# Kernel optimization log

Hardware: AMD Instinct MI355X
Metric: run time of the kernel (lower is better)

Reference implementation:

```python
import jax, jax.numpy as jnp
import numpy as np

COLOR_SIZE = 8
FILTERS = 128
L = 256 * 256 * 3  # flattened sequence length
EPS = 1e-12  # tf.math.l2_normalize epsilon


def setup_inputs() -> dict:
    key = jax.random.key(0)
    k1, k2, k3, k4, k5, k6 = jax.random.split(key, 6)
    example = jax.random.randint(k1, (4, 256, 256, 3), 0, COLOR_SIZE, dtype=jnp.int32)
    W_in = jax.random.normal(k2, (1, FILTERS), dtype=jnp.float32) * 0.05
    b_in = jnp.zeros((FILTERS,), dtype=jnp.float32)
    pos = jax.random.normal(k3, (L, FILTERS), dtype=jnp.float32) * 0.05
    W_final = jax.random.normal(k4, (FILTERS, COLOR_SIZE), dtype=jnp.float32) * 0.05
    b_final = jnp.zeros((COLOR_SIZE,), dtype=jnp.float32)
    return {"example": example, "W_in": W_in, "b_in": b_in, "pos": pos,
            "W_final": W_final, "b_final": b_final}


def reference(example, W_in, b_in, pos, W_final, b_final):
    B = example.shape[0]
    # cast + rescale to [-1, 1) (applied twice in the original code)
    x = example.astype(jnp.float32) / COLOR_SIZE * 2.0 - 1.0
    x = x.reshape(B, L, 1)
    x = x * 2.0 - 1.0
    # layer 0: Dense(1->F) + positional encoding + relu
    x = x * W_in[0] + b_in + pos  # [B, L, F]
    x = jax.nn.relu(x)
    # causal cumsum over sequence, then l2-normalize feature dim
    s = jnp.cumsum(x, axis=-2)  # [B, L, F]
    x = s * jax.lax.rsqrt(jnp.maximum(jnp.sum(s * s, axis=-1, keepdims=True), EPS))
    # final Dense(F->color_size)
    x = jnp.einsum('blf,fc->blc', x, W_final) + b_final
    return x.reshape(B, 256, 256, 3, COLOR_SIZE)
```

## Files before the change

### kernel.cpp

```cpp
#include <hip/hip_runtime.h>
#include <hip/hip_fp16.h>

#define BB   4
#define FF   128
#define CC   8
#define LSEQ 196608
#define NCH  2048
#define CL   96
#define TL   16
#define NT   6
#define NSEG 32
#define SEGL 64
#define TS   12

typedef _Float16 half8 __attribute__((ext_vector_type(8)));
typedef float    f32x4 __attribute__((ext_vector_type(4)));

__global__ __launch_bounds__(64) void k_chunksum(
    const int* __restrict__ ex, const float* __restrict__ W_in,
    const float* __restrict__ b_in, const float* __restrict__ pos,
    float* __restrict__ csum)
{
    __shared__ float xv[BB][CL];
    const int ch = blockIdx.x;
    const int t  = threadIdx.x;
    const int l0 = ch * CL;
    #pragma unroll
    for (int b = 0; b < BB; ++b)
        for (int i = t; i < CL; i += 64)
            xv[b][i] = (float)ex[(size_t)b * LSEQ + l0 + i] * 0.5f - 3.0f;
    __syncthreads();

    const float2 w  = *(const float2*)&W_in[2 * t];
    const float2 bb = *(const float2*)&b_in[2 * t];
    float2 s[BB];
    #pragma unroll
    for (int b = 0; b < BB; ++b) { s[b].x = 0.f; s[b].y = 0.f; }
    const float* pp = pos + (size_t)l0 * FF + 2 * t;
    #pragma unroll 4
    for (int l = 0; l < CL; ++l) {
        float2 p = *(const float2*)pp; pp += FF;
        float px = p.x + bb.x, py = p.y + bb.y;
        #pragma unroll
        for (int b = 0; b < BB; ++b) {
            float x = xv[b][l];
            s[b].x += fmaxf(fmaf(x, w.x, px), 0.f);
            s[b].y += fmaxf(fmaf(x, w.y, py), 0.f);
        }
    }
    #pragma unroll
    for (int b = 0; b < BB; ++b)
        *(float2*)&csum[((size_t)b * NCH + ch) * FF + 2 * t] = s[b];
}

__global__ __launch_bounds__(128) void k_segsum(
    const float* __restrict__ csum, float* __restrict__ segT)
{
    const int seg = blockIdx.x, b = blockIdx.y, f = threadIdx.x;
    const float* p = csum + ((size_t)b * NCH + (size_t)seg * SEGL) * FF + f;
    float a = 0.f;
    #pragma unroll 8
    for (int i = 0; i < SEGL; ++i) a += p[(size_t)i * FF];
    segT[((size_t)b * NSEG + seg) * FF + f] = a;
}

__global__ __launch_bounds__(128) void k_segscan(float* __restrict__ segT)
{
    const int b = blockIdx.x, f = threadIdx.x;
    float acc = 0.f;
    for (int s = 0; s < NSEG; ++s) {
        size_t idx = ((size_t)b * NSEG + s) * FF + f;
        float v = segT[idx];
        segT[idx] = acc;
        acc += v;
    }
}

__global__ __launch_bounds__(128) void k_chscan(
    float* __restrict__ csum, const float* __restrict__ segT)
{
    const int seg = blockIdx.x, b = blockIdx.y, f = threadIdx.x;
    float acc = segT[((size_t)b * NSEG + seg) * FF + f];
    float* p = csum + ((size_t)b * NCH + (size_t)seg * SEGL) * FF + f;
    #pragma unroll 8
    for (int i = 0; i < SEGL; ++i) {
        float v = p[(size_t)i * FF];
        p[(size_t)i * FF] = acc;
        acc += v;
    }
}

__global__ __launch_bounds__(256, 4) void k_final(
    const int* __restrict__ ex, const float* __restrict__ W_in,
    const float* __restrict__ b_in, const float* __restrict__ pos,
    const float* __restrict__ Wf, const float* __restrict__ bfin,
    const float* __restrict__ csum, float* __restrict__ out)
{
    __shared__ __align__(16) __half stile[BB][TL][FF];
    __shared__ __align__(16) float  tbuf[BB][TL][TS];

    const int ch   = blockIdx.x;
    const int l0   = ch * CL;
    const int t    = threadIdx.x;
    const int b    = __builtin_amdgcn_readfirstlane(t >> 6);
    const int lane = t & 63;
    const int lo   = lane & 15;
    const int hi   = lane >> 4;

    const int* exu = ex + (size_t)b * LSEQ + l0;

    half8 wfrag[4];
    #pragma unroll
    for (int kk = 0; kk < 4; ++kk) {
        #pragma unroll
        for (int j = 0; j < 8; ++j) {
            int k = kk * 32 + hi * 8 + j;
            float wv = (lo < CC) ? Wf[k * CC + lo] : 0.f;
            wfrag[kk][j] = (_Float16)wv;
        }
    }
    const f32x4 bf0 = *(const f32x4*)&bfin[0];
    const f32x4 bf1 = *(const f32x4*)&bfin[4];

    const float2 w  = *(const float2*)&W_in[2 * lane];
    const float2 bb = *(const float2*)&b_in[2 * lane];
    float2 s = *(const float2*)&csum[((size_t)b * NCH + ch) * FF + 2 * lane];

    char* sbase = (char*)&stile[b][0][0];
    const int ra0 = lo * 256 + ((hi * 16) ^ ((lo & 7) << 4));
    const int wa  = 4 * lane;

    const int jq = lo - 4 * hi;
    const bool isdiag = (jq >= 0) && (jq < 4);

    for (int tile = 0; tile < NT; ++tile) {
        const float* pp = pos + (size_t)(l0 + tile * TL) * FF + 2 * lane;
        #pragma unroll
        for (int l = 0; l < TL; ++l) {
            float2 p = *(const float2*)pp; pp += FF;
            float x = (float)exu[tile * TL + l] * 0.5f - 3.0f;
            s.x = fmaxf(fmaf(x, w.x, p.x + bb.x), 0.f) + s.x;
            s.y = fmaxf(fmaf(x, w.y, p.y + bb.y), 0.f) + s.y;
            __half2 h = __float22half2_rn(make_float2(s.x, s.y));
            *(__half2*)(sbase + l * 256 + (wa ^ ((l & 7) << 4))) = h;
        }

        f32x4 y  = {0.f, 0.f, 0.f, 0.f};
        f32x4 c2 = {0.f, 0.f, 0.f, 0.f};
        #pragma unroll
        for (int kk = 0; kk < 4; ++kk) {
            half8 a = *(half8*)(sbase + (ra0 ^ (kk << 6)));
            y  = __builtin_amdgcn_mfma_f32_16x16x32_f16(a, wfrag[kk], y, 0, 0, 0);
            c2 = __builtin_amdgcn_mfma_f32_16x16x32_f16(a, a,        c2, 0, 0, 0);
        }

        if (lo < CC) {
            tbuf[b][4 * hi + 0][lo] = y[0];
            tbuf[b][4 * hi + 1][lo] = y[1];
            tbuf[b][4 * hi + 2][lo] = y[2];
            tbuf[b][4 * hi + 3][lo] = y[3];
        }
        if (isdiag) {
            float qd = c2[0];
            qd = (jq == 1) ? c2[1] : qd;
            qd = (jq == 2) ? c2[2] : qd;
            qd = (jq == 3) ? c2[3] : qd;
            tbuf[b][lo][CC] = qd;
        }
        if (lane < TL) {
            const float* tr = &tbuf[b][lane][0];
            f32x4 v0 = *(const f32x4*)tr;
            f32x4 v1 = *(const f32x4*)(tr + 4);
            float rr = rsqrtf(fmaxf(tr[CC], 1e-12f));
            v0 = v0 * rr + bf0;
            v1 = v1 * rr + bf1;
            float* op = out + (((size_t)b * LSEQ) + l0 + tile * TL + lane) * CC;
            *(f32x4*)op       = v0;
            *(f32x4*)(op + 4) = v1;
        }
    }
}

extern "C" void kernel_launch(void* const* d_in, const int* in_sizes, int n_in,
                              void* d_out, int out_size, void* d_ws, size_t ws_size,
                              hipStream_t stream) {
    const int*   ex   = (const int*)d_in[0];
    const float* W_in = (const float*)d_in[1];
    const float* b_in = (const float*)d_in[2];
    const float* pos  = (const float*)d_in[3];
    const float* Wf   = (const float*)d_in[4];
    const float* bf   = (const float*)d_in[5];
    float* out  = (float*)d_out;
    float* csum = (float*)d_ws;
    float* segT = csum + (size_t)BB * NCH * FF;

    k_chunksum<<<NCH, 64, 0, stream>>>(ex, W_in, b_in, pos, csum);
    k_segsum  <<<dim3(NSEG, BB), 128, 0, stream>>>(csum, segT);
    k_segscan <<<BB, 128, 0, stream>>>(segT);
    k_chscan  <<<dim3(NSEG, BB), 128, 0, stream>>>(csum, segT);
    k_final   <<<NCH, 256, 0, stream>>>(ex, W_in, b_in, pos, Wf, bf, csum, out);
}
```

Measured before the change: 68.83 us.

## Share pos loads across batches in final kernel via per-wave sequence chunks

```diff
diff --git a/kernel.cpp b/kernel.cpp
--- a/kernel.cpp
+++ b/kernel.cpp
@@ -5,11 +5,11 @@
 #define FF   128
 #define CC   8
 #define LSEQ 196608
-#define NCH  2048
-#define CL   96
-#define TL   16
+#define NCH  8192
+#define CL   24
+#define TL   4
 #define NT   6
-#define NSEG 32
+#define NSEG 128
 #define SEGL 64
 #define TS   12
 
@@ -25,10 +25,11 @@
     const int ch = blockIdx.x;
     const int t  = threadIdx.x;
     const int l0 = ch * CL;
-    #pragma unroll
-    for (int b = 0; b < BB; ++b)
-        for (int i = t; i < CL; i += 64)
-            xv[b][i] = (float)ex[(size_t)b * LSEQ + l0 + i] * 0.5f - 3.0f;
+    if (t < CL) {
+        #pragma unroll
+        for (int b = 0; b < BB; ++b)
+            xv[b][t] = (float)ex[(size_t)b * LSEQ + l0 + t] * 0.5f - 3.0f;
+    }
     __syncthreads();
 
     const float2 w  = *(const float2*)&W_in[2 * t];
@@ -37,7 +38,7 @@
     #pragma unroll
     for (int b = 0; b < BB; ++b) { s[b].x = 0.f; s[b].y = 0.f; }
     const float* pp = pos + (size_t)l0 * FF + 2 * t;
-    #pragma unroll 4
+    #pragma unroll
     for (int l = 0; l < CL; ++l) {
         float2 p = *(const float2*)pp; pp += FF;
         float px = p.x + bb.x, py = p.y + bb.y;
@@ -96,18 +97,18 @@
     const float* __restrict__ Wf, const float* __restrict__ bfin,
     const float* __restrict__ csum, float* __restrict__ out)
 {
-    __shared__ __align__(16) __half stile[BB][TL][FF];
-    __shared__ __align__(16) float  tbuf[BB][TL][TS];
-
-    const int ch   = blockIdx.x;
-    const int l0   = ch * CL;
+    __shared__ __align__(16) __half stile[4][16][FF];
+    __shared__ __align__(16) float  tbuf[4][16][TS];
+
     const int t    = threadIdx.x;
-    const int b    = __builtin_amdgcn_readfirstlane(t >> 6);
+    const int wu   = __builtin_amdgcn_readfirstlane(t >> 6);
     const int lane = t & 63;
     const int lo   = lane & 15;
     const int hi   = lane >> 4;
-
-    const int* exu = ex + (size_t)b * LSEQ + l0;
+    const int ci   = blockIdx.x * 4 + wu;
+    const int l0   = ci * CL;
+
+    const int* ex0 = ex + l0;
 
     half8 wfrag[4];
     #pragma unroll
@@ -124,9 +125,12 @@
 
     const float2 w  = *(const float2*)&W_in[2 * lane];
     const float2 bb = *(const float2*)&b_in[2 * lane];
-    float2 s = *(const float2*)&csum[((size_t)b * NCH + ch) * FF + 2 * lane];
-
-    char* sbase = (char*)&stile[b][0][0];
+    float2 s[BB];
+    #pragma unroll
+    for (int b = 0; b < BB; ++b)
+        s[b] = *(const float2*)&csum[((size_t)b * NCH + ci) * FF + 2 * lane];
+
+    char* sbase = (char*)&stile[wu][0][0];
     const int ra0 = lo * 256 + ((hi * 16) ^ ((lo & 7) << 4));
     const int wa  = 4 * lane;
 
@@ -138,11 +142,16 @@
         #pragma unroll
         for (int l = 0; l < TL; ++l) {
             float2 p = *(const float2*)pp; pp += FF;
-            float x = (float)exu[tile * TL + l] * 0.5f - 3.0f;
-            s.x = fmaxf(fmaf(x, w.x, p.x + bb.x), 0.f) + s.x;
-            s.y = fmaxf(fmaf(x, w.y, p.y + bb.y), 0.f) + s.y;
-            __half2 h = __float22half2_rn(make_float2(s.x, s.y));
-            *(__half2*)(sbase + l * 256 + (wa ^ ((l & 7) << 4))) = h;
+            float px = p.x + bb.x, py = p.y + bb.y;
+            #pragma unroll
+            for (int b = 0; b < BB; ++b) {
+                float x = (float)ex0[b * LSEQ + tile * TL + l] * 0.5f - 3.0f;
+                s[b].x = fmaxf(fmaf(x, w.x, px), 0.f) + s[b].x;
+                s[b].y = fmaxf(fmaf(x, w.y, py), 0.f) + s[b].y;
+                __half2 h = __float22half2_rn(make_float2(s[b].x, s[b].y));
+                const int row = b * TL + l;
+                *(__half2*)(sbase + row * 256 + (wa ^ ((row & 7) << 4))) = h;
+            }
         }
 
         f32x4 y  = {0.f, 0.f, 0.f, 0.f};
@@ -155,26 +164,27 @@
         }
 
         if (lo < CC) {
-            tbuf[b][4 * hi + 0][lo] = y[0];
-            tbuf[b][4 * hi + 1][lo] = y[1];
-            tbuf[b][4 * hi + 2][lo] = y[2];
-            tbuf[b][4 * hi + 3][lo] = y[3];
+            tbuf[wu][4 * hi + 0][lo] = y[0];
+            tbuf[wu][4 * hi + 1][lo] = y[1];
+            tbuf[wu][4 * hi + 2][lo] = y[2];
+            tbuf[wu][4 * hi + 3][lo] = y[3];
         }
         if (isdiag) {
             float qd = c2[0];
             qd = (jq == 1) ? c2[1] : qd;
             qd = (jq == 2) ? c2[2] : qd;
             qd = (jq == 3) ? c2[3] : qd;
-            tbuf[b][lo][CC] = qd;
-        }
-        if (lane < TL) {
-            const float* tr = &tbuf[b][lane][0];
+            tbuf[wu][lo][CC] = qd;
+        }
+        if (lane < 16) {
+            const float* tr = &tbuf[wu][lane][0];
             f32x4 v0 = *(const f32x4*)tr;
             f32x4 v1 = *(const f32x4*)(tr + 4);
             float rr = rsqrtf(fmaxf(tr[CC], 1e-12f));
             v0 = v0 * rr + bf0;
             v1 = v1 * rr + bf1;
-            float* op = out + (((size_t)b * LSEQ) + l0 + tile * TL + lane) * CC;
+            const int b2 = lane >> 2, l2 = lane & 3;
+            float* op = out + ((size_t)b2 * LSEQ + l0 + tile * TL + l2) * CC;
             *(f32x4*)op       = v0;
             *(f32x4*)(op + 4) = v1;
         }
@@ -198,5 +208,5 @@
     k_segsum  <<<dim3(NSEG, BB), 128, 0, stream>>>(csum, segT);
     k_segscan <<<BB, 128, 0, stream>>>(segT);
     k_chscan  <<<dim3(NSEG, BB), 128, 0, stream>>>(csum, segT);
-    k_final   <<<NCH, 256, 0, stream>>>(ex, W_in, b_in, pos, Wf, bf, csum, out);
-}
+    k_final   <<<NCH / 4, 256, 0, stream>>>(ex, W_in, b_in, pos, Wf, bf, csum, out);
+}
```

Result: no change. 69.16 us (+0.5%).

## Fuse chunk-sum, scan and output into one persistent kernel with grid barriers

Applied to the files above, without the earlier changes.

```diff
diff --git a/kernel.cpp b/kernel.cpp
--- a/kernel.cpp
+++ b/kernel.cpp
@@ -5,109 +5,101 @@
 #define FF   128
 #define CC   8
 #define LSEQ 196608
-#define NCH  2048
-#define CL   96
+#define GRID 768
+#define CL   256
 #define TL   16
-#define NT   6
-#define NSEG 32
-#define SEGL 64
+#define NT   16
 #define TS   12
+#define CPL  12
 
 typedef _Float16 half8 __attribute__((ext_vector_type(8)));
 typedef float    f32x4 __attribute__((ext_vector_type(4)));
 
-__global__ __launch_bounds__(64) void k_chunksum(
-    const int* __restrict__ ex, const float* __restrict__ W_in,
-    const float* __restrict__ b_in, const float* __restrict__ pos,
-    float* __restrict__ csum)
-{
-    __shared__ float xv[BB][CL];
-    const int ch = blockIdx.x;
-    const int t  = threadIdx.x;
-    const int l0 = ch * CL;
-    #pragma unroll
-    for (int b = 0; b < BB; ++b)
-        for (int i = t; i < CL; i += 64)
-            xv[b][i] = (float)ex[(size_t)b * LSEQ + l0 + i] * 0.5f - 3.0f;
-    __syncthreads();
-
-    const float2 w  = *(const float2*)&W_in[2 * t];
-    const float2 bb = *(const float2*)&b_in[2 * t];
-    float2 s[BB];
-    #pragma unroll
-    for (int b = 0; b < BB; ++b) { s[b].x = 0.f; s[b].y = 0.f; }
-    const float* pp = pos + (size_t)l0 * FF + 2 * t;
-    #pragma unroll 4
-    for (int l = 0; l < CL; ++l) {
-        float2 p = *(const float2*)pp; pp += FF;
-        float px = p.x + bb.x, py = p.y + bb.y;
-        #pragma unroll
-        for (int b = 0; b < BB; ++b) {
-            float x = xv[b][l];
-            s[b].x += fmaxf(fmaf(x, w.x, px), 0.f);
-            s[b].y += fmaxf(fmaf(x, w.y, py), 0.f);
-        }
-    }
-    #pragma unroll
-    for (int b = 0; b < BB; ++b)
-        *(float2*)&csum[((size_t)b * NCH + ch) * FF + 2 * t] = s[b];
+__global__ __launch_bounds__(64) void k_zero(int* ctr) {
+    if (threadIdx.x < 2) ctr[threadIdx.x] = 0;
 }
 
-__global__ __launch_bounds__(128) void k_segsum(
-    const float* __restrict__ csum, float* __restrict__ segT)
-{
-    const int seg = blockIdx.x, b = blockIdx.y, f = threadIdx.x;
-    const float* p = csum + ((size_t)b * NCH + (size_t)seg * SEGL) * FF + f;
-    float a = 0.f;
-    #pragma unroll 8
-    for (int i = 0; i < SEGL; ++i) a += p[(size_t)i * FF];
-    segT[((size_t)b * NSEG + seg) * FF + f] = a;
+static __device__ __forceinline__ void gridbar(int* ctr) {
+    __syncthreads();
+    if (threadIdx.x == 0) {
+        __threadfence();
+        atomicAdd(ctr, 1);
+        while (atomicAdd(ctr, 0) < GRID) __builtin_amdgcn_s_sleep(2);
+        __threadfence();
+    }
+    __syncthreads();
 }
 
-__global__ __launch_bounds__(128) void k_segscan(float* __restrict__ segT)
-{
-    const int b = blockIdx.x, f = threadIdx.x;
-    float acc = 0.f;
-    for (int s = 0; s < NSEG; ++s) {
-        size_t idx = ((size_t)b * NSEG + s) * FF + f;
-        float v = segT[idx];
-        segT[idx] = acc;
-        acc += v;
-    }
-}
-
-__global__ __launch_bounds__(128) void k_chscan(
-    float* __restrict__ csum, const float* __restrict__ segT)
-{
-    const int seg = blockIdx.x, b = blockIdx.y, f = threadIdx.x;
-    float acc = segT[((size_t)b * NSEG + seg) * FF + f];
-    float* p = csum + ((size_t)b * NCH + (size_t)seg * SEGL) * FF + f;
-    #pragma unroll 8
-    for (int i = 0; i < SEGL; ++i) {
-        float v = p[(size_t)i * FF];
-        p[(size_t)i * FF] = acc;
-        acc += v;
-    }
-}
-
-__global__ __launch_bounds__(256, 4) void k_final(
+__global__ __launch_bounds__(256, 3) void k_fused(
     const int* __restrict__ ex, const float* __restrict__ W_in,
     const float* __restrict__ b_in, const float* __restrict__ pos,
     const float* __restrict__ Wf, const float* __restrict__ bfin,
-    const float* __restrict__ csum, float* __restrict__ out)
+    int* __restrict__ ctr, float* __restrict__ csum, float* __restrict__ out)
 {
-    __shared__ __align__(16) __half stile[BB][TL][FF];
-    __shared__ __align__(16) float  tbuf[BB][TL][TS];
+    __shared__ __align__(16) __half stile[4][TL][FF];
+    __shared__ __align__(16) float  tbuf[4][TL][TS];
 
-    const int ch   = blockIdx.x;
-    const int l0   = ch * CL;
     const int t    = threadIdx.x;
-    const int b    = __builtin_amdgcn_readfirstlane(t >> 6);
+    const int wu   = __builtin_amdgcn_readfirstlane(t >> 6);
     const int lane = t & 63;
     const int lo   = lane & 15;
     const int hi   = lane >> 4;
+    const int ch   = blockIdx.x;
+    const int l0   = ch * CL;
 
-    const int* exu = ex + (size_t)b * LSEQ + l0;
+    const float2 w  = *(const float2*)&W_in[2 * lane];
+    const float2 bb = *(const float2*)&b_in[2 * lane];
+    const int* exu = ex + (size_t)wu * LSEQ + l0;
+
+    float* cp = &csum[((size_t)wu * GRID + ch) * FF + 2 * lane];
+    {
+        float2 a = {0.f, 0.f};
+        const float* pp = pos + (size_t)l0 * FF + 2 * lane;
+        #pragma unroll 4
+        for (int l = 0; l < CL; ++l) {
+            float2 p = *(const float2*)pp; pp += FF;
+            float x = (float)exu[l] * 0.5f - 3.0f;
+            a.x += fmaxf(fmaf(x, w.x, p.x + bb.x), 0.f);
+            a.y += fmaxf(fmaf(x, w.y, p.y + bb.y), 0.f);
+        }
+        atomicExch(cp,     a.x);
+        atomicExch(cp + 1, a.y);
+    }
+
+    gridbar(&ctr[0]);
+
+    if (blockIdx.x < 64) {
+        const int sid = blockIdx.x * 4 + wu;
+        const int b   = sid >> 6;
+        const int fp  = sid & 63;
+        float* base = csum + (size_t)b * GRID * FF + 2 * fp;
+        float2 vals[CPL];
+        float2 tot = {0.f, 0.f};
+        #pragma unroll
+        for (int i = 0; i < CPL; ++i) {
+            float* p = base + (size_t)(lane * CPL + i) * FF;
+            vals[i].x = atomicAdd(p,     0.f);
+            vals[i].y = atomicAdd(p + 1, 0.f);
+            tot.x += vals[i].x; tot.y += vals[i].y;
+        }
+        float vx = tot.x, vy = tot.y;
+        #pragma unroll
+        for (int d = 1; d < 64; d <<= 1) {
+            float ux = __shfl_up(vx, d);
+            float uy = __shfl_up(vy, d);
+            if (lane >= d) { vx += ux; vy += uy; }
+        }
+        float2 excl = {vx - tot.x, vy - tot.y};
+        #pragma unroll
+        for (int i = 0; i < CPL; ++i) {
+            float* p = base + (size_t)(lane * CPL + i) * FF;
+            atomicExch(p,     excl.x);
+            atomicExch(p + 1, excl.y);
+            excl.x += vals[i].x; excl.y += vals[i].y;
+        }
+    }
+
+    gridbar(&ctr[1]);
 
     half8 wfrag[4];
     #pragma unroll
@@ -122,14 +114,13 @@
     const f32x4 bf0 = *(const f32x4*)&bfin[0];
     const f32x4 bf1 = *(const f32x4*)&bfin[4];
 
-    const float2 w  = *(const float2*)&W_in[2 * lane];
-    const float2 bb = *(const float2*)&b_in[2 * lane];
-    float2 s = *(const float2*)&csum[((size_t)b * NCH + ch) * FF + 2 * lane];
+    float2 s;
+    s.x = atomicAdd(cp,     0.f);
+    s.y = atomicAdd(cp + 1, 0.f);
 
-    char* sbase = (char*)&stile[b][0][0];
+    char* sbase = (char*)&stile[wu][0][0];
     const int ra0 = lo * 256 + ((hi * 16) ^ ((lo & 7) << 4));
     const int wa  = 4 * lane;
-
     const int jq = lo - 4 * hi;
     const bool isdiag = (jq >= 0) && (jq < 4);
 
@@ -155,26 +146,26 @@
         }
 
         if (lo < CC) {
-            tbuf[b][4 * hi + 0][lo] = y[0];
-            tbuf[b][4 * hi + 1][lo] = y[1];
-            tbuf[b][4 * hi + 2][lo] = y[2];
-            tbuf[b][4 * hi + 3][lo] = y[3];
+            tbuf[wu][4 * hi + 0][lo] = y[0];
+            tbuf[wu][4 * hi + 1][lo] = y[1];
+            tbuf[wu][4 * hi + 2][lo] = y[2];
+            tbuf[wu][4 * hi + 3][lo] = y[3];
         }
         if (isdiag) {
             float qd = c2[0];
             qd = (jq == 1) ? c2[1] : qd;
             qd = (jq == 2) ? c2[2] : qd;
             qd = (jq == 3) ? c2[3] : qd;
-            tbuf[b][lo][CC] = qd;
+            tbuf[wu][lo][CC] = qd;
         }
         if (lane < TL) {
-            const float* tr = &tbuf[b][lane][0];
+            const float* tr = &tbuf[wu][lane][0];
             f32x4 v0 = *(const f32x4*)tr;
             f32x4 v1 = *(const f32x4*)(tr + 4);
             float rr = rsqrtf(fmaxf(tr[CC], 1e-12f));
             v0 = v0 * rr + bf0;
             v1 = v1 * rr + bf1;
-            float* op = out + (((size_t)b * LSEQ) + l0 + tile * TL + lane) * CC;
+            float* op = out + ((size_t)wu * LSEQ + l0 + tile * TL + lane) * CC;
             *(f32x4*)op       = v0;
             *(f32x4*)(op + 4) = v1;
         }
@@ -191,12 +182,9 @@
     const float* Wf   = (const float*)d_in[4];
     const float* bf   = (const float*)d_in[5];
     float* out  = (float*)d_out;
-    float* csum = (float*)d_ws;
-    float* segT = csum + (size_t)BB * NCH * FF;
+    int*   ctr  = (int*)d_ws;
+    float* csum = (float*)((char*)d_ws + 256);
 
-    k_chunksum<<<NCH, 64, 0, stream>>>(ex, W_in, b_in, pos, csum);
-    k_segsum  <<<dim3(NSEG, BB), 128, 0, stream>>>(csum, segT);
-    k_segscan <<<BB, 128, 0, stream>>>(segT);
-    k_chscan  <<<dim3(NSEG, BB), 128, 0, stream>>>(csum, segT);
-    k_final   <<<NCH, 256, 0, stream>>>(ex, W_in, b_in, pos, Wf, bf, csum, out);
+    k_zero<<<1, 64, 0, stream>>>(ctr);
+    k_fused<<<GRID, 256, 0, stream>>>(ex, W_in, b_in, pos, Wf, bf, ctr, csum, out);
 }
```

After: 253.6 us. +268.5%, slower.
